# Performance work log

Measured on AMD Instinct MI355X. Metric: run time of the kernel, lower is better.

Reference implementation:

```python
import jax, jax.numpy as jnp
import numpy as np

B, L, H = 32, 2048, 512


def setup_inputs() -> dict:
    key = jax.random.key(0)
    k1, k2, k3, k4, k5, k6 = jax.random.split(key, 6)
    scale = 1.0 / np.sqrt(H)
    return {
        "query": jax.random.normal(k1, (B, H), dtype=jnp.float32),
        "ref": jax.random.normal(k2, (B, L, H), dtype=jnp.float32),
        "mask": jax.random.randint(k3, (B, L), 0, 2) == 1,
        # learned params (torch Linear weight layout: [out, in]; apply as x @ W.T)
        "W_ref": jax.random.normal(k4, (H, H), dtype=jnp.float32) * scale,
        "W_q": jax.random.normal(k5, (H, H), dtype=jnp.float32) * scale,
        "v": jax.random.normal(k6, (H,), dtype=jnp.float32) * scale,
    }


def reference(query, ref, mask, W_ref, W_q, v):
    scale = 1.0 / np.sqrt(H)
    # additive (Bahdanau) scores: v^T tanh(W_ref ref + W_q q)
    encoded_ref = jnp.einsum("blh,oh->blo", ref, W_ref)          # (B, L, H)
    encoded_q = jnp.einsum("bh,oh->bo", query, W_q)[:, None, :]  # (B, 1, H)
    scores = jnp.einsum("blh,h->bl", jnp.tanh(encoded_ref + encoded_q), v)
    scores = scores * scale
    scores = jnp.where(mask, -1e9, scores)
    attn = jax.nn.softmax(scores, axis=1)                         # (B, L)
    glimpse = jnp.einsum("bl,blh->bh", attn, ref)                 # (B, H)
    return glimpse, scores
```

## Files before the change

### kernel.cpp

```cpp
#include <hip/hip_runtime.h>
#include <hip/hip_bf16.h>
#include <cstdint>

typedef __attribute__((ext_vector_type(4))) float f32x4;
typedef __attribute__((ext_vector_type(8))) short s16x8;

#define NB   32
#define NL   2048
#define NH   512
#define NM   (NB * NL)
#define SCALE 0.04419417382415922f
#define LDST 40

__device__ __forceinline__ ushort f2bf(float f) {
    union { float f; unsigned u; } a; a.f = f;
    unsigned u = a.u;
    unsigned r = (u + 0x7FFFu + ((u >> 16) & 1u)) >> 16;
    return (ushort)r;
}

__global__ __launch_bounds__(256) void k_convW(const float* __restrict__ W,
                                               ushort* __restrict__ Wb) {
    int i = blockIdx.x * 256 + threadIdx.x;
    const float4* s = (const float4*)W;
    float4 a = s[2 * i], c = s[2 * i + 1];
    union { ushort u[8]; int4 v; } p;
    p.u[0] = f2bf(a.x); p.u[1] = f2bf(a.y); p.u[2] = f2bf(a.z); p.u[3] = f2bf(a.w);
    p.u[4] = f2bf(c.x); p.u[5] = f2bf(c.y); p.u[6] = f2bf(c.z); p.u[7] = f2bf(c.w);
    ((int4*)Wb)[i] = p.v;
}

__global__ __launch_bounds__(512) void k_eq(const float* __restrict__ query,
                                            const float* __restrict__ Wq,
                                            float* __restrict__ eq) {
    int b = blockIdx.x;
    int o = threadIdx.x;
    __shared__ float q[NH];
    q[o] = query[b * NH + o];
    __syncthreads();
    const float4* w = (const float4*)(Wq + (size_t)o * NH);
    float acc = 0.f;
#pragma unroll 4
    for (int i = 0; i < NH / 4; ++i) {
        float4 x = w[i];
        acc += q[4 * i] * x.x + q[4 * i + 1] * x.y + q[4 * i + 2] * x.z + q[4 * i + 3] * x.w;
    }
    eq[b * NH + o] = acc;
}

__global__ __launch_bounds__(256) void k_gemm(const float* __restrict__ ref,
                                              const ushort* __restrict__ Wb,
                                              const float* __restrict__ eq,
                                              const float* __restrict__ v,
                                              float* __restrict__ part) {
    __shared__ ushort As[128 * LDST];
    __shared__ ushort Bs[128 * LDST];

    int tid = threadIdx.x;
    int lane = tid & 63, wid = tid >> 6;
    int wr = wid >> 1, wc = wid & 1;

    int phys = blockIdx.x;
    int xcd = phys & 7, slot = phys >> 3;
    int mt = xcd * 64 + (slot >> 2);
    int nt = slot & 3;
    int m0 = mt * 128, n0 = nt * 128;
    int b = mt >> 4;

    f32x4 acc[4][4];
#pragma unroll
    for (int i = 0; i < 4; ++i)
#pragma unroll
        for (int j = 0; j < 4; ++j) acc[i][j] = (f32x4)(0.f);

    int srow = tid >> 1, sks = (tid & 1) * 16;
    const float*  asrc = ref + (size_t)(m0 + srow) * NH + sks;
    const ushort* bsrc = Wb + (size_t)(n0 + srow) * NH + sks;
    int awr = srow * LDST + sks;

    int lr = lane & 15, kq = lane >> 4;
    int aoff[4], boff[4];
#pragma unroll
    for (int f = 0; f < 4; ++f) {
        aoff[f] = (wr * 64 + f * 16 + lr) * LDST + kq * 8;
        boff[f] = (wc * 64 + f * 16 + lr) * LDST + kq * 8;
    }

    for (int kt = 0; kt < 16; ++kt) {
        __syncthreads();
        {
            const float* s = asrc + kt * 32;
            float4 f0 = *(const float4*)(s);
            float4 f1 = *(const float4*)(s + 4);
            float4 f2 = *(const float4*)(s + 8);
            float4 f3 = *(const float4*)(s + 12);
            union { ushort u[8]; int4 v; } p0, p1;
            p0.u[0] = f2bf(f0.x); p0.u[1] = f2bf(f0.y); p0.u[2] = f2bf(f0.z); p0.u[3] = f2bf(f0.w);
            p0.u[4] = f2bf(f1.x); p0.u[5] = f2bf(f1.y); p0.u[6] = f2bf(f1.z); p0.u[7] = f2bf(f1.w);
            p1.u[0] = f2bf(f2.x); p1.u[1] = f2bf(f2.y); p1.u[2] = f2bf(f2.z); p1.u[3] = f2bf(f2.w);
            p1.u[4] = f2bf(f3.x); p1.u[5] = f2bf(f3.y); p1.u[6] = f2bf(f3.z); p1.u[7] = f2bf(f3.w);
            *(int4*)&As[awr] = p0.v;
            *(int4*)&As[awr + 8] = p1.v;
            const int4* bs = (const int4*)(bsrc + kt * 32);
            *(int4*)&Bs[awr] = bs[0];
            *(int4*)&Bs[awr + 8] = bs[1];
        }
        __syncthreads();
        s16x8 af[4], bf[4];
#pragma unroll
        for (int f = 0; f < 4; ++f) af[f] = *(const s16x8*)&As[aoff[f]];
#pragma unroll
        for (int f = 0; f < 4; ++f) bf[f] = *(const s16x8*)&Bs[boff[f]];
#pragma unroll
        for (int fr = 0; fr < 4; ++fr)
#pragma unroll
            for (int fc = 0; fc < 4; ++fc)
                acc[fr][fc] = __builtin_amdgcn_mfma_f32_16x16x32_bf16(
                    af[fr], bf[fc], acc[fr][fc], 0, 0, 0);
    }

    const float* eqb = eq + b * NH;
    float vv[4], ee[4];
#pragma unroll
    for (int fc = 0; fc < 4; ++fc) {
        int c = n0 + wc * 64 + fc * 16 + lr;
        vv[fc] = v[c];
        ee[fc] = eqb[c];
    }
#pragma unroll
    for (int fr = 0; fr < 4; ++fr) {
#pragma unroll
        for (int reg = 0; reg < 4; ++reg) {
            float s = 0.f;
#pragma unroll
            for (int fc = 0; fc < 4; ++fc) {
                float x = acc[fr][fc][reg] + ee[fc];
                float t = 1.f - 2.f / (__expf(2.f * x) + 1.f);
                s += vv[fc] * t;
            }
            s += __shfl_xor(s, 1);
            s += __shfl_xor(s, 2);
            s += __shfl_xor(s, 4);
            s += __shfl_xor(s, 8);
            if (lr == 0) {
                int row = wr * 64 + fr * 16 + kq * 4 + reg;
                part[(size_t)nt * NM + m0 + row] = s;
            }
        }
    }
}

__global__ __launch_bounds__(256) void k_softmax(const float* __restrict__ part,
                                                 const int* __restrict__ mask,
                                                 float* __restrict__ out_sc,
                                                 float* __restrict__ attn) {
    int b = blockIdx.x;
    int tid = threadIdx.x;
    int lane = tid & 63, wid = tid >> 6;
    __shared__ float red[4];
    float sc[8];
    float mx = -3.4e38f;
#pragma unroll
    for (int i = 0; i < 8; ++i) {
        int m = b * NL + i * 256 + tid;
        float s = (part[m] + part[NM + m] + part[2 * NM + m] + part[3 * NM + m]) * SCALE;
        if (mask[m] != 0) s = -1e9f;
        out_sc[m] = s;
        sc[i] = s;
        mx = fmaxf(mx, s);
    }
#pragma unroll
    for (int o = 32; o >= 1; o >>= 1) mx = fmaxf(mx, __shfl_xor(mx, o));
    if (lane == 0) red[wid] = mx;
    __syncthreads();
    mx = fmaxf(fmaxf(red[0], red[1]), fmaxf(red[2], red[3]));
    __syncthreads();
    float ls = 0.f;
#pragma unroll
    for (int i = 0; i < 8; ++i) {
        float e = __expf(sc[i] - mx);
        sc[i] = e;
        ls += e;
    }
#pragma unroll
    for (int o = 32; o >= 1; o >>= 1) ls += __shfl_xor(ls, o);
    if (lane == 0) red[wid] = ls;
    __syncthreads();
    float inv = 1.f / (red[0] + red[1] + red[2] + red[3]);
#pragma unroll
    for (int i = 0; i < 8; ++i) attn[b * NL + i * 256 + tid] = sc[i] * inv;
}

__global__ __launch_bounds__(256) void k_glp(const float* __restrict__ ref,
                                             const float* __restrict__ attn,
                                             float* __restrict__ glp) {
    int sp = blockIdx.x, b = blockIdx.y;
    int tid = threadIdx.x;
    const float* attb = attn + b * NL + sp * 128;
    float2 acc = make_float2(0.f, 0.f);
#pragma unroll 4
    for (int l = 0; l < 128; ++l) {
        float a = attb[l];
        const float2* row = (const float2*)(ref + (size_t)(b * NL + sp * 128 + l) * NH);
        float2 r = row[tid];
        acc.x += a * r.x;
        acc.y += a * r.y;
    }
    ((float2*)(glp + (size_t)(sp * NB + b) * NH))[tid] = acc;
}

__global__ __launch_bounds__(256) void k_gred(const float* __restrict__ glp,
                                              float* __restrict__ out_gl) {
    int idx = blockIdx.x * 256 + threadIdx.x;
    float s = 0.f;
#pragma unroll
    for (int sp = 0; sp < 16; ++sp) s += glp[sp * (NB * NH) + idx];
    out_gl[idx] = s;
}

extern "C" void kernel_launch(void* const* d_in, const int* in_sizes, int n_in,
                              void* d_out, int out_size, void* d_ws, size_t ws_size,
                              hipStream_t stream) {
    const float* query = (const float*)d_in[0];
    const float* ref   = (const float*)d_in[1];
    const int*   mask  = (const int*)d_in[2];
    const float* W_ref = (const float*)d_in[3];
    const float* W_q   = (const float*)d_in[4];
    const float* v     = (const float*)d_in[5];

    float* out_gl = (float*)d_out;
    float* out_sc = out_gl + NB * NH;

    char* w = (char*)d_ws;
    ushort* wW  = (ushort*)w;
    float* eq   = (float*)(w + 524288);
    float* part = (float*)(w + 589824);
    float* attn = (float*)(w + 1638400);
    float* glp  = (float*)(w + 1900544);

    k_convW<<<128, 256, 0, stream>>>(W_ref, wW);
    k_eq<<<NB, 512, 0, stream>>>(query, W_q, eq);
    k_gemm<<<2048, 256, 0, stream>>>(ref, wW, eq, v, part);
    k_softmax<<<NB, 256, 0, stream>>>(part, mask, out_sc, attn);
    k_glp<<<dim3(16, NB), 256, 0, stream>>>(ref, attn, glp);
    k_gred<<<64, 256, 0, stream>>>(glp, out_gl);
}
```

Baseline: 139.2 us.

## Prefetch next K-tile into registers and change LDS padding in GEMM

```diff
diff --git a/kernel.cpp b/kernel.cpp
--- a/kernel.cpp
+++ b/kernel.cpp
@@ -10,13 +10,11 @@
 #define NH   512
 #define NM   (NB * NL)
 #define SCALE 0.04419417382415922f
-#define LDST 40
+#define LDST 36
 
 __device__ __forceinline__ ushort f2bf(float f) {
-    union { float f; unsigned u; } a; a.f = f;
-    unsigned u = a.u;
-    unsigned r = (u + 0x7FFFu + ((u >> 16) & 1u)) >> 16;
-    return (ushort)r;
+    __hip_bfloat16 b = __float2bfloat16(f);
+    return *reinterpret_cast<ushort*>(&b);
 }
 
 __global__ __launch_bounds__(256) void k_convW(const float* __restrict__ W,
@@ -86,31 +84,49 @@
         boff[f] = (wc * 64 + f * 16 + lr) * LDST + kq * 8;
     }
 
+    float4 pa0, pa1, pa2, pa3;
+    int4 pb0, pb1;
+    {
+        const float* s = asrc;
+        pa0 = *(const float4*)(s);
+        pa1 = *(const float4*)(s + 4);
+        pa2 = *(const float4*)(s + 8);
+        pa3 = *(const float4*)(s + 12);
+        const int4* bs = (const int4*)(bsrc);
+        pb0 = bs[0];
+        pb1 = bs[1];
+    }
+
     for (int kt = 0; kt < 16; ++kt) {
+        union { ushort u[8]; int4 v; } p0, p1;
+        p0.u[0] = f2bf(pa0.x); p0.u[1] = f2bf(pa0.y); p0.u[2] = f2bf(pa0.z); p0.u[3] = f2bf(pa0.w);
+        p0.u[4] = f2bf(pa1.x); p0.u[5] = f2bf(pa1.y); p0.u[6] = f2bf(pa1.z); p0.u[7] = f2bf(pa1.w);
+        p1.u[0] = f2bf(pa2.x); p1.u[1] = f2bf(pa2.y); p1.u[2] = f2bf(pa2.z); p1.u[3] = f2bf(pa2.w);
+        p1.u[4] = f2bf(pa3.x); p1.u[5] = f2bf(pa3.y); p1.u[6] = f2bf(pa3.z); p1.u[7] = f2bf(pa3.w);
+        *(int4*)&As[awr] = p0.v;
+        *(int4*)&As[awr + 8] = p1.v;
+        *(int4*)&Bs[awr] = pb0;
+        *(int4*)&Bs[awr + 8] = pb1;
         __syncthreads();
-        {
-            const float* s = asrc + kt * 32;
-            float4 f0 = *(const float4*)(s);
-            float4 f1 = *(const float4*)(s + 4);
-            float4 f2 = *(const float4*)(s + 8);
-            float4 f3 = *(const float4*)(s + 12);
-            union { ushort u[8]; int4 v; } p0, p1;
-            p0.u[0] = f2bf(f0.x); p0.u[1] = f2bf(f0.y); p0.u[2] = f2bf(f0.z); p0.u[3] = f2bf(f0.w);
-            p0.u[4] = f2bf(f1.x); p0.u[5] = f2bf(f1.y); p0.u[6] = f2bf(f1.z); p0.u[7] = f2bf(f1.w);
-            p1.u[0] = f2bf(f2.x); p1.u[1] = f2bf(f2.y); p1.u[2] = f2bf(f2.z); p1.u[3] = f2bf(f2.w);
-            p1.u[4] = f2bf(f3.x); p1.u[5] = f2bf(f3.y); p1.u[6] = f2bf(f3.z); p1.u[7] = f2bf(f3.w);
-            *(int4*)&As[awr] = p0.v;
-            *(int4*)&As[awr + 8] = p1.v;
-            const int4* bs = (const int4*)(bsrc + kt * 32);
-            *(int4*)&Bs[awr] = bs[0];
-            *(int4*)&Bs[awr + 8] = bs[1];
+
+        if (kt < 15) {
+            const float* s = asrc + (kt + 1) * 32;
+            pa0 = *(const float4*)(s);
+            pa1 = *(const float4*)(s + 4);
+            pa2 = *(const float4*)(s + 8);
+            pa3 = *(const float4*)(s + 12);
+            const int4* bs = (const int4*)(bsrc + (kt + 1) * 32);
+            pb0 = bs[0];
+            pb1 = bs[1];
         }
+
+        s16x8 af[4], bf[4];
+#pragma unroll
+        for (int f = 0; f < 4; ++f) af[f] = *(const s16x8*)&As[aoff[f]];
+#pragma unroll
+        for (int f = 0; f < 4; ++f) bf[f] = *(const s16x8*)&Bs[boff[f]];
         __syncthreads();
-        s16x8 af[4], bf[4];
-#pragma unroll
-        for (int f = 0; f < 4; ++f) af[f] = *(const s16x8*)&As[aoff[f]];
-#pragma unroll
-        for (int f = 0; f < 4; ++f) bf[f] = *(const s16x8*)&Bs[boff[f]];
+
 #pragma unroll
         for (int fr = 0; fr < 4; ++fr)
 #pragma unroll
```

Measured after the change: 128.6 us. -7.7%, faster.

## Double-buffer GEMM shared tiles with register prefetch of next K tile

Applied to the files above, without the earlier changes.

```diff
diff --git a/kernel.cpp b/kernel.cpp
--- a/kernel.cpp
+++ b/kernel.cpp
@@ -10,13 +10,12 @@
 #define NH   512
 #define NM   (NB * NL)
 #define SCALE 0.04419417382415922f
-#define LDST 40
+#define LDST 36
+#define BUFO (128 * LDST)
 
 __device__ __forceinline__ ushort f2bf(float f) {
-    union { float f; unsigned u; } a; a.f = f;
-    unsigned u = a.u;
-    unsigned r = (u + 0x7FFFu + ((u >> 16) & 1u)) >> 16;
-    return (ushort)r;
+    __hip_bfloat16 b = __float2bfloat16(f);
+    return *reinterpret_cast<ushort*>(&b);
 }
 
 __global__ __launch_bounds__(256) void k_convW(const float* __restrict__ W,
@@ -53,8 +52,8 @@
                                               const float* __restrict__ eq,
                                               const float* __restrict__ v,
                                               float* __restrict__ part) {
-    __shared__ ushort As[128 * LDST];
-    __shared__ ushort Bs[128 * LDST];
+    __shared__ ushort As[2 * BUFO];
+    __shared__ ushort Bs[2 * BUFO];
 
     int tid = threadIdx.x;
     int lane = tid & 63, wid = tid >> 6;
@@ -86,37 +85,67 @@
         boff[f] = (wc * 64 + f * 16 + lr) * LDST + kq * 8;
     }
 
-    for (int kt = 0; kt < 16; ++kt) {
+#define LOAD_TILE(kt)                                          \
+    {   const float* s_ = asrc + (kt) * 32;                    \
+        pa0 = *(const float4*)(s_);                            \
+        pa1 = *(const float4*)(s_ + 4);                        \
+        pa2 = *(const float4*)(s_ + 8);                        \
+        pa3 = *(const float4*)(s_ + 12);                       \
+        const int4* bs_ = (const int4*)(bsrc + (kt) * 32);     \
+        pb0 = bs_[0];                                          \
+        pb1 = bs_[1]; }
+
+#define WRITE_TILE(AB, BB)                                                                         \
+    {   union { ushort u[8]; int4 v; } p0, p1;                                                     \
+        p0.u[0] = f2bf(pa0.x); p0.u[1] = f2bf(pa0.y); p0.u[2] = f2bf(pa0.z); p0.u[3] = f2bf(pa0.w);\
+        p0.u[4] = f2bf(pa1.x); p0.u[5] = f2bf(pa1.y); p0.u[6] = f2bf(pa1.z); p0.u[7] = f2bf(pa1.w);\
+        p1.u[0] = f2bf(pa2.x); p1.u[1] = f2bf(pa2.y); p1.u[2] = f2bf(pa2.z); p1.u[3] = f2bf(pa2.w);\
+        p1.u[4] = f2bf(pa3.x); p1.u[5] = f2bf(pa3.y); p1.u[6] = f2bf(pa3.z); p1.u[7] = f2bf(pa3.w);\
+        *(int4*)&(AB)[awr] = p0.v;                                                                 \
+        *(int4*)&(AB)[awr + 8] = p1.v;                                                             \
+        *(int4*)&(BB)[awr] = pb0;                                                                  \
+        *(int4*)&(BB)[awr + 8] = pb1; }
+
+#define READ_FRAGS(AB, BB)                                      \
+    _Pragma("unroll")                                           \
+    for (int f = 0; f < 4; ++f) af[f] = *(const s16x8*)&(AB)[aoff[f]]; \
+    _Pragma("unroll")                                           \
+    for (int f = 0; f < 4; ++f) bf[f] = *(const s16x8*)&(BB)[boff[f]];
+
+#define DO_MFMA()                                               \
+    _Pragma("unroll")                                           \
+    for (int fr = 0; fr < 4; ++fr)                              \
+        _Pragma("unroll")                                       \
+        for (int fc = 0; fc < 4; ++fc)                          \
+            acc[fr][fc] = __builtin_amdgcn_mfma_f32_16x16x32_bf16(af[fr], bf[fc], acc[fr][fc], 0, 0, 0);
+
+    float4 pa0, pa1, pa2, pa3;
+    int4 pb0, pb1;
+
+    LOAD_TILE(0)
+    WRITE_TILE(As, Bs)
+    __syncthreads();
+
+    for (int kt2 = 0; kt2 < 8; ++kt2) {
+        s16x8 af[4], bf[4];
+        LOAD_TILE(2 * kt2 + 1)
+        READ_FRAGS(As, Bs)
+        DO_MFMA()
+        __builtin_amdgcn_sched_barrier(0);
+        WRITE_TILE(As + BUFO, Bs + BUFO)
         __syncthreads();
-        {
-            const float* s = asrc + kt * 32;
-            float4 f0 = *(const float4*)(s);
-            float4 f1 = *(const float4*)(s + 4);
-            float4 f2 = *(const float4*)(s + 8);
-            float4 f3 = *(const float4*)(s + 12);
-            union { ushort u[8]; int4 v; } p0, p1;
-            p0.u[0] = f2bf(f0.x); p0.u[1] = f2bf(f0.y); p0.u[2] = f2bf(f0.z); p0.u[3] = f2bf(f0.w);
-            p0.u[4] = f2bf(f1.x); p0.u[5] = f2bf(f1.y); p0.u[6] = f2bf(f1.z); p0.u[7] = f2bf(f1.w);
-            p1.u[0] = f2bf(f2.x); p1.u[1] = f2bf(f2.y); p1.u[2] = f2bf(f2.z); p1.u[3] = f2bf(f2.w);
-            p1.u[4] = f2bf(f3.x); p1.u[5] = f2bf(f3.y); p1.u[6] = f2bf(f3.z); p1.u[7] = f2bf(f3.w);
-            *(int4*)&As[awr] = p0.v;
-            *(int4*)&As[awr + 8] = p1.v;
-            const int4* bs = (const int4*)(bsrc + kt * 32);
-            *(int4*)&Bs[awr] = bs[0];
-            *(int4*)&Bs[awr + 8] = bs[1];
+
+        if (kt2 < 7) {
+            LOAD_TILE(2 * kt2 + 2)
+            READ_FRAGS(As + BUFO, Bs + BUFO)
+            DO_MFMA()
+            __builtin_amdgcn_sched_barrier(0);
+            WRITE_TILE(As, Bs)
+            __syncthreads();
+        } else {
+            READ_FRAGS(As + BUFO, Bs + BUFO)
+            DO_MFMA()
         }
-        __syncthreads();
-        s16x8 af[4], bf[4];
-#pragma unroll
-        for (int f = 0; f < 4; ++f) af[f] = *(const s16x8*)&As[aoff[f]];
-#pragma unroll
-        for (int f = 0; f < 4; ++f) bf[f] = *(const s16x8*)&Bs[boff[f]];
-#pragma unroll
-        for (int fr = 0; fr < 4; ++fr)
-#pragma unroll
-            for (int fc = 0; fc < 4; ++fc)
-                acc[fr][fc] = __builtin_amdgcn_mfma_f32_16x16x32_bf16(
-                    af[fr], bf[fc], acc[fr][fc], 0, 0, 0);
     }
 
     const float* eqb = eq + b * NH;
```

Result: slower. 143.0 us (+2.7%).
